# Kernel tuning notes

Measured on AMD Instinct MI355X. Metric: run time of the kernel, lower is better.

## Reference

```python
import jax, jax.numpy as jnp
import numpy as np

N_NODES = 4096
N_EDGES = 32768
IN_FEAT = 256
OUT_FEAT = 128
HID = 64
IN_HEAD = 64
OUT_HEAD = 5
NEG_SLOPE = 0.2
EPS = 1e-16


def setup_inputs() -> dict:
    key = jax.random.key(0)
    ks = jax.random.split(key, 12)
    x = jax.random.normal(ks[0], (N_NODES, IN_FEAT), dtype=jnp.float32)
    src = jax.random.randint(ks[1], (N_EDGES,), 0, N_NODES)
    dst = jax.random.randint(ks[2], (N_EDGES,), 0, N_NODES)
    edge_index = jnp.stack([src, dst]).astype(jnp.int64)
    s1 = 1.0 / np.sqrt(IN_FEAT)
    s2 = 1.0 / np.sqrt(HID * IN_HEAD)
    W1 = jax.random.normal(ks[3], (IN_FEAT, IN_HEAD * HID), dtype=jnp.float32) * s1
    att_src1 = jax.random.normal(ks[4], (IN_HEAD, HID), dtype=jnp.float32) * 0.1
    att_dst1 = jax.random.normal(ks[5], (IN_HEAD, HID), dtype=jnp.float32) * 0.1
    b1 = jnp.zeros((IN_HEAD * HID,), dtype=jnp.float32)
    W2 = jax.random.normal(ks[6], (IN_HEAD * HID, OUT_HEAD * OUT_FEAT), dtype=jnp.float32) * s2
    att_src2 = jax.random.normal(ks[7], (OUT_HEAD, OUT_FEAT), dtype=jnp.float32) * 0.1
    att_dst2 = jax.random.normal(ks[8], (OUT_HEAD, OUT_FEAT), dtype=jnp.float32) * 0.1
    b2 = jnp.zeros((OUT_FEAT,), dtype=jnp.float32)
    return {"x": x, "edge_index": edge_index, "W1": W1, "att_src1": att_src1,
            "att_dst1": att_dst1, "b1": b1, "W2": W2, "att_src2": att_src2,
            "att_dst2": att_dst2, "b2": b2}


def _gat_conv(x, W, att_src, att_dst, bias, src, dst, heads, out_c, concat):
    # x: [N, F_in]; returns [N, heads*out_c] (concat) or [N, out_c] (mean)
    n = x.shape[0]
    h = (x @ W).reshape(n, heads, out_c)                       # [N,H,C]
    a_src = jnp.sum(h * att_src, axis=-1)                      # [N,H]
    a_dst = jnp.sum(h * att_dst, axis=-1)                      # [N,H]
    e = jax.nn.leaky_relu(a_src[src] + a_dst[dst], NEG_SLOPE)  # [E,H]
    # segment softmax over edges grouped by destination node (PyG softmax)
    m = jax.ops.segment_max(e, dst, num_segments=n)            # [N,H]
    ex = jnp.exp(e - m[dst])
    denom = jax.ops.segment_sum(ex, dst, num_segments=n)       # [N,H]
    alpha = ex / (denom[dst] + EPS)                            # [E,H]
    out = jax.ops.segment_sum(alpha[:, :, None] * h[src], dst, num_segments=n)  # [N,H,C]
    out = out.reshape(n, heads * out_c) if concat else out.mean(axis=1)
    return out + bias


def reference(x, edge_index, W1, att_src1, att_dst1, b1, W2, att_src2, att_dst2, b2):
    n = x.shape[0]
    # PyG GATConv default: add self loops
    loop = jnp.arange(n, dtype=edge_index.dtype)
    src = jnp.concatenate([edge_index[0], loop])
    dst = jnp.concatenate([edge_index[1], loop])
    # dropout layers are identity in eval mode
    h = _gat_conv(x, W1, att_src1, att_dst1, b1, src, dst, IN_HEAD, HID, True)
    h = jax.nn.elu(h)
    h = _gat_conv(h, W2, att_src2, att_dst2, b2, src, dst, OUT_HEAD, OUT_FEAT, False)
    s = jnp.mean(h, axis=0)
    return jnp.tanh(s)
```

## Files before the change

### kernel.cpp

```cpp
#include <hip/hip_runtime.h>
#include <hip/hip_bf16.h>

#define N_NODES 4096
#define NE      32768
#define E_TOT   (NE + N_NODES)
#define IN_FEAT 256
#define HID     64
#define IN_HEAD 64
#define F1      4096
#define OUT_HEAD 5
#define OUT_FEAT 128
#define F2      640
#define NEG_SLOPE 0.2f
#define EPS_A   1e-16f

typedef __bf16 bf16;
typedef bf16 bf16x8 __attribute__((ext_vector_type(8)));
typedef bf16 bf16x4 __attribute__((ext_vector_type(4)));
typedef float f32x4 __attribute__((ext_vector_type(4)));

__device__ inline void async_cp16(bf16* lds, const bf16* g) {
    __builtin_amdgcn_global_load_lds(
        (const __attribute__((address_space(1))) unsigned int*)g,
        (__attribute__((address_space(3))) unsigned int*)lds, 16, 0, 0);
}

__global__ void hist_kernel(const int* __restrict__ edst, int* counts) {
    int e = blockIdx.x * 256 + threadIdx.x;
    if (e >= E_TOT) return;
    int d = (e < NE) ? edst[e] : (e - NE);
    atomicAdd(&counts[d], 1);
}

__global__ void scan_kernel(const int* __restrict__ counts,
                            int* __restrict__ row_start, int* __restrict__ cursor) {
    __shared__ int part[256];
    __shared__ int pre[257];
    int t = threadIdx.x;
    int base = t * 16;
    int local[16];
    int s = 0;
#pragma unroll
    for (int i = 0; i < 16; ++i) { local[i] = s; s += counts[base + i]; }
    part[t] = s;
    __syncthreads();
    if (t == 0) {
        int r = 0;
        for (int i = 0; i < 256; ++i) { pre[i] = r; r += part[i]; }
        pre[256] = r;
    }
    __syncthreads();
    int off = pre[t];
#pragma unroll
    for (int i = 0; i < 16; ++i) {
        int v = off + local[i];
        row_start[base + i] = v;
        cursor[base + i] = v;
    }
    if (t == 0) row_start[N_NODES] = pre[256];
}

__global__ void scatter_kernel(const int* __restrict__ esrc,
                               const int* __restrict__ edst,
                               int* cursor, int* __restrict__ srclist) {
    int e = blockIdx.x * 256 + threadIdx.x;
    if (e >= E_TOT) return;
    int d = (e < NE) ? edst[e] : (e - NE);
    int s = (e < NE) ? esrc[e] : (e - NE);
    int slot = atomicAdd(&cursor[d], 1);
    srclist[slot] = s;
}

#define PB_X   512
#define PB_W1  1024
#define PB_W2  2560
__global__ __launch_bounds__(256)
void prep_kernel(const float* __restrict__ x, bf16* __restrict__ xb,
                 const float* __restrict__ W1, bf16* __restrict__ W1T,
                 const float* __restrict__ W2, bf16* __restrict__ W2T,
                 const float* __restrict__ as1, const float* __restrict__ ad1,
                 bf16* __restrict__ w1s, bf16* __restrict__ w1d) {
    __shared__ float tile[32][33];
    int b = blockIdx.x, t = threadIdx.x;
    if (b < PB_X) {
        int i = b * 256 + t;
        f32x4 a = *(const f32x4*)(x + (size_t)i * 8);
        f32x4 c = *(const f32x4*)(x + (size_t)i * 8 + 4);
        bf16x8 r;
        r[0] = (bf16)a[0]; r[1] = (bf16)a[1]; r[2] = (bf16)a[2]; r[3] = (bf16)a[3];
        r[4] = (bf16)c[0]; r[5] = (bf16)c[1]; r[6] = (bf16)c[2]; r[7] = (bf16)c[3];
        *(bf16x8*)(xb + (size_t)i * 8) = r;
    } else if (b < PB_X + PB_W1 + PB_W2) {
        const float* S; bf16* D; int R, C, gx, gy;
        if (b < PB_X + PB_W1) {
            int bb = b - PB_X;
            S = W1; D = W1T; R = IN_FEAT; C = F1;
            gx = bb % (F1 / 32); gy = bb / (F1 / 32);
        } else {
            int bb = b - PB_X - PB_W1;
            S = W2; D = W2T; R = F1; C = F2;
            gx = bb % (F2 / 32); gy = bb / (F2 / 32);
        }
        int tx = t & 31, ty = t >> 5;
        int c0 = gx * 32, r0 = gy * 32;
#pragma unroll
        for (int i = 0; i < 4; ++i)
            tile[ty + i * 8][tx] = S[(size_t)(r0 + ty + i * 8) * C + c0 + tx];
        __syncthreads();
#pragma unroll
        for (int i = 0; i < 4; ++i)
            D[(size_t)(c0 + ty + i * 8) * R + r0 + tx] = (bf16)tile[tx][ty + i * 8];
    } else {
        int id = (b - PB_X - PB_W1 - PB_W2) * 256 + t;
        int k = id >> 6, h = id & 63;
        const float* wrow = W1 + (size_t)k * F1 + h * HID;
        const float* a1 = as1 + h * HID;
        const float* a2 = ad1 + h * HID;
        float s = 0.f, d = 0.f;
#pragma unroll 8
        for (int c = 0; c < HID; ++c) {
            float w = wrow[c];
            s += w * a1[c];
            d += w * a2[c];
        }
        w1s[id] = (bf16)s;
        w1d[id] = (bf16)d;
    }
}

template <int SPLITK, bool SWZ, typename TC>
__global__ __launch_bounds__(256)
void gemm128_kernel(const bf16* __restrict__ A, const bf16* __restrict__ BT,
                    TC* __restrict__ C, int M, int N, int K) {
    __shared__ bf16 As[128][64];
    __shared__ bf16 Bs[128][64];
    const int tid  = threadIdx.x;
    const int wave = tid >> 6, lane = tid & 63;
    const int quad = lane >> 4, lr = lane & 15;
    int nb, mb, zb;
    if constexpr (SWZ) {
        int bid = blockIdx.x;
        int xx = bid & 7, q = bid >> 3;
        int gp = q / 5; nb = q - gp * 5;
        int g = gp * 8 + xx;
        mb = g >> 2; zb = g & 3;
    } else {
        nb = blockIdx.x; mb = blockIdx.y; zb = blockIdx.z;
    }
    const int m0 = mb * 128, n0 = nb * 128;
    const int kchunk = K / SPLITK;
    const int kbeg = zb * kchunk;
    const int wm = (wave >> 1) * 64;
    const int wn = (wave & 1) * 64;
    TC* Cz = C + (size_t)zb * M * N;

    const int srow = lane >> 3;
    const int scol = ((lane & 7) ^ srow) * 8;
    const int xk = lr & 7;

    f32x4 acc[4][4] = {};

    for (int kk = 0; kk < kchunk; kk += 64) {
        int k0 = kbeg + kk;
#pragma unroll
        for (int c = 0; c < 4; ++c) {
            int r = wave * 32 + c * 8;
            async_cp16(&As[r][0], A + (size_t)(m0 + r + srow) * K + k0 + scol);
            async_cp16(&Bs[r][0], BT + (size_t)(n0 + r + srow) * K + k0 + scol);
        }
        __syncthreads();

#pragma unroll
        for (int ks = 0; ks < 2; ++ks) {
            int ch = ((ks * 4 + quad) ^ xk) * 8;
            bf16x8 af[4], bfr[4];
#pragma unroll
            for (int mt = 0; mt < 4; ++mt)
                af[mt] = *(const bf16x8*)(&As[wm + mt * 16 + lr][ch]);
#pragma unroll
            for (int nt = 0; nt < 4; ++nt)
                bfr[nt] = *(const bf16x8*)(&Bs[wn + nt * 16 + lr][ch]);
#pragma unroll
            for (int mt = 0; mt < 4; ++mt)
#pragma unroll
                for (int nt = 0; nt < 4; ++nt)
                    acc[mt][nt] = __builtin_amdgcn_mfma_f32_16x16x32_bf16(
                        af[mt], bfr[nt], acc[mt][nt], 0, 0, 0);
        }
        __syncthreads();
    }

#pragma unroll
    for (int mt = 0; mt < 4; ++mt)
#pragma unroll
        for (int nt = 0; nt < 4; ++nt) {
            int row0 = m0 + wm + mt * 16 + quad * 4;
            int col = n0 + wn + nt * 16 + lr;
#pragma unroll
            for (int r = 0; r < 4; ++r)
                Cz[(size_t)(row0 + r) * N + col] = (TC)acc[mt][nt][r];
        }
}

__global__ __launch_bounds__(256)
void gemv1_kernel(const float* __restrict__ x,
                  const bf16* __restrict__ w1s, const bf16* __restrict__ w1d,
                  float* __restrict__ a_src, float* __restrict__ a_dst) {
    int wave = threadIdx.x >> 6, lane = threadIdx.x & 63;
    int n = blockIdx.x * 4 + wave;
    const float* xr = x + (size_t)n * IN_FEAT;
    float s = 0.f, d = 0.f;
    for (int k0 = 0; k0 < IN_FEAT; k0 += 4) {
        f32x4 xv = *(const f32x4*)(xr + k0);
#pragma unroll
        for (int j = 0; j < 4; ++j) {
            float xs = xv[j];
            s += xs * (float)w1s[(k0 + j) * IN_HEAD + lane];
            d += xs * (float)w1d[(k0 + j) * IN_HEAD + lane];
        }
    }
    a_src[n * IN_HEAD + lane] = s;
    a_dst[n * IN_HEAD + lane] = d;
}

__global__ __launch_bounds__(64)
void agg1_kernel(const int* __restrict__ row_start,
                 const int* __restrict__ srclist,
                 const float* __restrict__ a_src, const float* __restrict__ a_dst,
                 const bf16* __restrict__ H1, const float* __restrict__ b1,
                 bf16* __restrict__ h_elu) {
    int bid = blockIdx.x;
    int c = bid & 7;
    int d = bid >> 3;
    int lane = threadIdx.x;
    int gh = c * 8 + (lane >> 3);
    int beg = row_start[d], deg = row_start[d + 1] - beg;
    float adst = a_dst[d * IN_HEAD + gh];
    int fbase = c * 512 + lane * 8;
    const float* asg = a_src + gh;

    auto SL = [&](int i) { return srclist[beg + (i < deg ? i : deg - 1)]; };

    int s0 = SL(0);
    int s1 = SL(1);
    float la0 = asg[(size_t)s0 * IN_HEAD];
    bf16x8 v0 = *(const bf16x8*)(H1 + (size_t)s0 * F1 + fbase);
    float la1 = asg[(size_t)s1 * IN_HEAD];
    bf16x8 v1 = *(const bf16x8*)(H1 + (size_t)s1 * F1 + fbase);
    int s2 = SL(2);

    float m = -1e30f, den = 0.f;
    float acc[8] = {};
    for (int i = 0; i < deg; ++i) {
        int s3 = SL(i + 3);
        float la2 = asg[(size_t)s2 * IN_HEAD];
        bf16x8 v2 = *(const bf16x8*)(H1 + (size_t)s2 * F1 + fbase);

        float l = la0 + adst;
        l = l > 0.f ? l : NEG_SLOPE * l;
        if (l > m + 12.f) {
            float r = __expf(m - l);
            den *= r;
#pragma unroll
            for (int k = 0; k < 8; ++k) acc[k] *= r;
            m = l;
        }
        float w = __expf(l - m);
        den += w;
#pragma unroll
        for (int k = 0; k < 8; ++k) acc[k] += w * (float)v0[k];

        la0 = la1; v0 = v1;
        la1 = la2; v1 = v2;
        s2 = s3;
    }
    float dinv = 1.f / (den + EPS_A);

    bf16x8 o;
#pragma unroll
    for (int j = 0; j < 8; ++j) {
        float v = acc[j] * dinv + b1[fbase + j];
        o[j] = (bf16)(v > 0.f ? v : (__expf(v) - 1.f));
    }
    *(bf16x8*)(h_elu + (size_t)d * F1 + fbase) = o;
}

__global__ __launch_bounds__(192)
void fold2_kernel(const bf16* __restrict__ Hp,
                  const float* __restrict__ as2, const float* __restrict__ ad2,
                  float* __restrict__ H2,
                  float* __restrict__ a_src, float* __restrict__ a_dst) {
    int n = blockIdx.x, t = threadIdx.x;
    if (t >= 160) return;
    int h = t >> 5;
    f32x4 sum = {};
#pragma unroll
    for (int z = 0; z < 4; ++z) {
        bf16x4 v = *(const bf16x4*)(Hp + (size_t)z * N_NODES * F2 + (size_t)n * F2 + t * 4);
        sum[0] += (float)v[0]; sum[1] += (float)v[1];
        sum[2] += (float)v[2]; sum[3] += (float)v[3];
    }
    *(f32x4*)(H2 + (size_t)n * F2 + t * 4) = sum;
    f32x4 ws = *(const f32x4*)(as2 + t * 4);
    f32x4 wd = *(const f32x4*)(ad2 + t * 4);
    float s = sum[0] * ws[0] + sum[1] * ws[1] + sum[2] * ws[2] + sum[3] * ws[3];
    float d = sum[0] * wd[0] + sum[1] * wd[1] + sum[2] * wd[2] + sum[3] * wd[3];
#pragma unroll
    for (int o = 1; o <= 16; o <<= 1) {
        s += __shfl_xor(s, o);
        d += __shfl_xor(d, o);
    }
    if ((t & 31) == 0) {
        a_src[n * OUT_HEAD + h] = s;
        a_dst[n * OUT_HEAD + h] = d;
    }
}

__global__ void stats2_kernel(const int* __restrict__ row_start,
                              const int* __restrict__ srclist,
                              const float* __restrict__ a_src,
                              const float* __restrict__ a_dst,
                              float* __restrict__ beta) {
    int id = blockIdx.x * 256 + threadIdx.x;
    if (id >= N_NODES * OUT_HEAD) return;
    int d = id / OUT_HEAD, h = id - d * OUT_HEAD;
    int beg = row_start[d], deg = row_start[d + 1] - beg;
    float adst = a_dst[id];
    float m = -1e30f, den = 0.f;
    for (int i = 0; i < deg; ++i) {
        int s = srclist[beg + i];
        float l = a_src[s * OUT_HEAD + h] + adst;
        l = l > 0.f ? l : NEG_SLOPE * l;
        if (l > m) { den = den * __expf(m - l) + 1.f; m = l; }
        else den += __expf(l - m);
    }
    float dinv = 1.f / (den + EPS_A);
    for (int i = 0; i < deg; ++i) {
        int s = srclist[beg + i];
        float l = a_src[s * OUT_HEAD + h] + adst;
        l = l > 0.f ? l : NEG_SLOPE * l;
        atomicAdd(&beta[s * OUT_HEAD + h], __expf(l - m) * dinv);
    }
}

__global__ __launch_bounds__(256)
void wsum_kernel(const float* __restrict__ H2, const float* __restrict__ beta,
                 float* __restrict__ acc_out, const float* __restrict__ b2,
                 float* __restrict__ out, int* __restrict__ ticket) {
    __shared__ float buf[F2];
    __shared__ int lastblk;
    int t = threadIdx.x;
    int n0 = blockIdx.x * 32;
    int h = t >> 5;
    float a0 = 0.f, a1 = 0.f, a2 = 0.f, a3 = 0.f;
    if (t < 160) {
        for (int i = 0; i < 32; ++i) {
            int s = n0 + i;
            float bh = beta[s * OUT_HEAD + h];
            f32x4 v = *(const f32x4*)(H2 + (size_t)s * F2 + t * 4);
            a0 += bh * v[0]; a1 += bh * v[1];
            a2 += bh * v[2]; a3 += bh * v[3];
        }
        buf[t * 4 + 0] = a0; buf[t * 4 + 1] = a1;
        buf[t * 4 + 2] = a2; buf[t * 4 + 3] = a3;
    }
    __syncthreads();
    if (t < OUT_FEAT) {
        float s = 0.f;
#pragma unroll
        for (int hh = 0; hh < OUT_HEAD; ++hh) s += buf[hh * OUT_FEAT + t];
        atomicAdd(&acc_out[(blockIdx.x & 7) * OUT_FEAT + t], s);
    }
    __syncthreads();
    if (t == 0) {
        __threadfence();
        lastblk = (atomicAdd(ticket, 1) == (int)gridDim.x - 1);
    }
    __syncthreads();
    if (lastblk && t < OUT_FEAT) {
        float tot = 0.f;
#pragma unroll
        for (int k = 0; k < 8; ++k)
            tot += atomicAdd(&acc_out[k * OUT_FEAT + t], 0.0f);
        out[t] = tanhf(tot * (1.f / (OUT_HEAD * (float)N_NODES)) + b2[t]);
    }
}

extern "C" void kernel_launch(void* const* d_in, const int* in_sizes, int n_in,
                              void* d_out, int out_size, void* d_ws, size_t ws_size,
                              hipStream_t stream) {
    const float* x        = (const float*)d_in[0];
    const int*   ei       = (const int*)d_in[1];
    const float* W1       = (const float*)d_in[2];
    const float* att_src1 = (const float*)d_in[3];
    const float* att_dst1 = (const float*)d_in[4];
    const float* b1       = (const float*)d_in[5];
    const float* W2       = (const float*)d_in[6];
    const float* att_src2 = (const float*)d_in[7];
    const float* att_dst2 = (const float*)d_in[8];
    const float* b2       = (const float*)d_in[9];
    float* out = (float*)d_out;

    const int* esrc = ei;
    const int* edst = ei + NE;

    char* p = (char*)d_ws;
    auto bump = [&](size_t bytes) {
        void* r = (void*)p;
        p += (bytes + 255) & ~(size_t)255;
        return r;
    };
    bf16*  H1     = (bf16*)bump((size_t)N_NODES * F1 * 2);
    bf16*  h_elu  = (bf16*)bump((size_t)N_NODES * F1 * 2);
    float* H2     = (float*)bump((size_t)N_NODES * F2 * 4);
    bf16*  xb     = (bf16*)bump((size_t)N_NODES * IN_FEAT * 2);
    bf16*  W1T    = (bf16*)bump((size_t)F1 * IN_FEAT * 2);
    bf16*  W2T    = (bf16*)bump((size_t)F2 * F1 * 2);
    bf16*  w1s    = (bf16*)bump((size_t)IN_FEAT * IN_HEAD * 2);
    bf16*  w1d    = (bf16*)bump((size_t)IN_FEAT * IN_HEAD * 2);
    float* a_src1 = (float*)bump((size_t)N_NODES * IN_HEAD * 4);
    float* a_dst1 = (float*)bump((size_t)N_NODES * IN_HEAD * 4);
    float* a_src2 = (float*)bump((size_t)N_NODES * OUT_HEAD * 4);
    float* a_dst2 = (float*)bump((size_t)N_NODES * OUT_HEAD * 4);
    int*   row_start = (int*)bump((N_NODES + 1) * 4);
    int*   cursor  = (int*)bump(N_NODES * 4);
    int*   srclist = (int*)bump(E_TOT * 4);
    size_t zbytes = N_NODES * 4 + N_NODES * OUT_HEAD * 4 + 8 * OUT_FEAT * 4 + 4;
    int*   counts = (int*)bump(zbytes);
    float* beta    = (float*)((char*)counts + N_NODES * 4);
    float* acc_out = beta + N_NODES * OUT_HEAD;
    int*   ticket  = (int*)(acc_out + 8 * OUT_FEAT);
    bf16* Hp = H1;

    hipMemsetAsync(counts, 0, zbytes, stream);

    hist_kernel<<<(E_TOT + 255) / 256, 256, 0, stream>>>(edst, counts);
    scan_kernel<<<1, 256, 0, stream>>>(counts, row_start, cursor);
    scatter_kernel<<<(E_TOT + 255) / 256, 256, 0, stream>>>(
        esrc, edst, cursor, srclist);

    prep_kernel<<<PB_X + PB_W1 + PB_W2 + 64, 256, 0, stream>>>(
        x, xb, W1, W1T, W2, W2T, att_src1, att_dst1, w1s, w1d);

    gemm128_kernel<1, false, bf16>
        <<<dim3(F1 / 128, N_NODES / 128, 1), 256, 0, stream>>>(
        xb, W1T, H1, N_NODES, F1, IN_FEAT);
    gemv1_kernel<<<N_NODES / 4, 256, 0, stream>>>(x, w1s, w1d, a_src1, a_dst1);
    agg1_kernel<<<N_NODES * 8, 64, 0, stream>>>(
        row_start, srclist, a_src1, a_dst1, H1, b1, h_elu);

    gemm128_kernel<4, true, bf16><<<640, 256, 0, stream>>>(
        h_elu, W2T, Hp, N_NODES, F2, F1);
    fold2_kernel<<<N_NODES, 192, 0, stream>>>(
        Hp, att_src2, att_dst2, H2, a_src2, a_dst2);
    stats2_kernel<<<(N_NODES * OUT_HEAD + 255) / 256, 256, 0, stream>>>(
        row_start, srclist, a_src2, a_dst2, beta);
    wsum_kernel<<<N_NODES / 32, 256, 0, stream>>>(
        H2, beta, acc_out, b2, out, ticket);
}
```

Baseline: 240.3 us.

## Deepen agg1 prefetch pipeline and split layer-2 beta scatter into edge-parallel kernel

The layer-1 aggregation loop now keeps four neighbor rows and their attention logits in flight instead of two, hiding more gather latency. The layer-2 stats kernel now only computes per-node max and inverse denominator. A new edge-parallel kernel recomputes each edge's attention weight and atomically accumulates beta, replacing the serial second pass that ran per (node, head) thread. The deeper prefetch costs more registers, and the split adds a kernel launch and reads the edge arrays directly.

```diff
diff --git a/kernel.cpp b/kernel.cpp
--- a/kernel.cpp
+++ b/kernel.cpp
@@ -241,20 +241,23 @@
 
     auto SL = [&](int i) { return srclist[beg + (i < deg ? i : deg - 1)]; };
 
-    int s0 = SL(0);
-    int s1 = SL(1);
+    int s0 = SL(0), s1 = SL(1), s2 = SL(2), s3 = SL(3);
     float la0 = asg[(size_t)s0 * IN_HEAD];
     bf16x8 v0 = *(const bf16x8*)(H1 + (size_t)s0 * F1 + fbase);
     float la1 = asg[(size_t)s1 * IN_HEAD];
     bf16x8 v1 = *(const bf16x8*)(H1 + (size_t)s1 * F1 + fbase);
-    int s2 = SL(2);
+    float la2 = asg[(size_t)s2 * IN_HEAD];
+    bf16x8 v2 = *(const bf16x8*)(H1 + (size_t)s2 * F1 + fbase);
+    float la3 = asg[(size_t)s3 * IN_HEAD];
+    bf16x8 v3 = *(const bf16x8*)(H1 + (size_t)s3 * F1 + fbase);
+    int s4 = SL(4), s5 = SL(5);
 
     float m = -1e30f, den = 0.f;
     float acc[8] = {};
     for (int i = 0; i < deg; ++i) {
-        int s3 = SL(i + 3);
-        float la2 = asg[(size_t)s2 * IN_HEAD];
-        bf16x8 v2 = *(const bf16x8*)(H1 + (size_t)s2 * F1 + fbase);
+        int sn = SL(i + 6);
+        float la4 = asg[(size_t)s4 * IN_HEAD];
+        bf16x8 v4 = *(const bf16x8*)(H1 + (size_t)s4 * F1 + fbase);
 
         float l = la0 + adst;
         l = l > 0.f ? l : NEG_SLOPE * l;
@@ -272,7 +275,9 @@
 
         la0 = la1; v0 = v1;
         la1 = la2; v1 = v2;
-        s2 = s3;
+        la2 = la3; v2 = v3;
+        la3 = la4; v3 = v4;
+        s4 = s5; s5 = sn;
     }
     float dinv = 1.f / (den + EPS_A);
 
@@ -320,7 +325,7 @@
                               const int* __restrict__ srclist,
                               const float* __restrict__ a_src,
                               const float* __restrict__ a_dst,
-                              float* __restrict__ beta) {
+                              float* __restrict__ m2, float* __restrict__ dinv2) {
     int id = blockIdx.x * 256 + threadIdx.x;
     if (id >= N_NODES * OUT_HEAD) return;
     int d = id / OUT_HEAD, h = id - d * OUT_HEAD;
@@ -334,13 +339,23 @@
         if (l > m) { den = den * __expf(m - l) + 1.f; m = l; }
         else den += __expf(l - m);
     }
-    float dinv = 1.f / (den + EPS_A);
-    for (int i = 0; i < deg; ++i) {
-        int s = srclist[beg + i];
-        float l = a_src[s * OUT_HEAD + h] + adst;
-        l = l > 0.f ? l : NEG_SLOPE * l;
-        atomicAdd(&beta[s * OUT_HEAD + h], __expf(l - m) * dinv);
-    }
+    m2[id] = m;
+    dinv2[id] = 1.f / (den + EPS_A);
+}
+
+__global__ void beta_kernel(const int* __restrict__ es, const int* __restrict__ ed,
+                            const float* __restrict__ a_src, const float* __restrict__ a_dst,
+                            const float* __restrict__ m2, const float* __restrict__ dinv2,
+                            float* __restrict__ beta) {
+    int id = blockIdx.x * 256 + threadIdx.x;
+    if (id >= E_TOT * OUT_HEAD) return;
+    int e = id / OUT_HEAD, h = id - e * OUT_HEAD;
+    int s = (e < NE) ? es[e] : (e - NE);
+    int d = (e < NE) ? ed[e] : (e - NE);
+    float l = a_src[s * OUT_HEAD + h] + a_dst[d * OUT_HEAD + h];
+    l = l > 0.f ? l : NEG_SLOPE * l;
+    float alpha = __expf(l - m2[d * OUT_HEAD + h]) * dinv2[d * OUT_HEAD + h];
+    atomicAdd(&beta[s * OUT_HEAD + h], alpha);
 }
 
 __global__ __launch_bounds__(256)
@@ -422,6 +437,8 @@
     float* a_dst1 = (float*)bump((size_t)N_NODES * IN_HEAD * 4);
     float* a_src2 = (float*)bump((size_t)N_NODES * OUT_HEAD * 4);
     float* a_dst2 = (float*)bump((size_t)N_NODES * OUT_HEAD * 4);
+    float* m2     = (float*)bump((size_t)N_NODES * OUT_HEAD * 4);
+    float* dinv2  = (float*)bump((size_t)N_NODES * OUT_HEAD * 4);
     int*   row_start = (int*)bump((N_NODES + 1) * 4);
     int*   cursor  = (int*)bump(N_NODES * 4);
     int*   srclist = (int*)bump(E_TOT * 4);
@@ -454,7 +471,9 @@
     fold2_kernel<<<N_NODES, 192, 0, stream>>>(
         Hp, att_src2, att_dst2, H2, a_src2, a_dst2);
     stats2_kernel<<<(N_NODES * OUT_HEAD + 255) / 256, 256, 0, stream>>>(
-        row_start, srclist, a_src2, a_dst2, beta);
+        row_start, srclist, a_src2, a_dst2, m2, dinv2);
+    beta_kernel<<<(E_TOT * OUT_HEAD + 255) / 256, 256, 0, stream>>>(
+        esrc, edst, a_src2, a_dst2, m2, dinv2, beta);
     wsum_kernel<<<N_NODES / 32, 256, 0, stream>>>(
         H2, beta, acc_out, b2, out, ticket);
 }
```

After: 238.6 us. About the same (-0.7%).
